# Kernel optimization log

Measured on AMD Instinct MI355X. Metric: run time of the kernel, lower is better.

Reference implementation:

```python
import jax, jax.numpy as jnp
import numpy as np

B, S, D, H, DK, DV = 4, 1024, 1024, 16, 64, 64
NEG = -1e9  # matches torch masked_fill(-1000000000.0)


def setup_inputs() -> dict:
    key = jax.random.key(0)
    ks = jax.random.split(key, 12)
    scale = 1.0 / np.sqrt(D)
    return {
        "querys": jax.random.normal(ks[0], (B, S, D), jnp.float32),
        "keys": jax.random.normal(ks[1], (B, S, D), jnp.float32),
        "values": jax.random.normal(ks[2], (B, S, D), jnp.float32),
        "mask": jax.random.randint(ks[3], (S, S), 0, 2, jnp.int32),
        # stacked per-head projection params (nn.Linear style: y = x @ W^T + b -> here W stored as [D, dk])
        "Wq": jax.random.normal(ks[4], (H, D, DK), jnp.float32) * scale,
        "bq": jax.random.normal(ks[5], (H, DK), jnp.float32) * 0.01,
        "Wk": jax.random.normal(ks[6], (H, D, DK), jnp.float32) * scale,
        "bk": jax.random.normal(ks[7], (H, DK), jnp.float32) * 0.01,
        "Wv": jax.random.normal(ks[8], (H, D, DV), jnp.float32) * scale,
        "bv": jax.random.normal(ks[9], (H, DV), jnp.float32) * 0.01,
        "Wp": jax.random.normal(ks[10], (H * DV, D), jnp.float32) * (1.0 / np.sqrt(H * DV)),
        "bp": jax.random.normal(ks[11], (D,), jnp.float32) * 0.01,
    }


def reference(querys, keys, values, mask, Wq, bq, Wk, bk, Wv, bv, Wp, bp):
    # per-head projections, all heads batched: [B, H, S, dk/dv]
    q = jnp.einsum('bsd,hdk->bhsk', querys, Wq) + bq[None, :, None, :]
    k = jnp.einsum('bsd,hdk->bhsk', keys, Wk) + bk[None, :, None, :]
    v = jnp.einsum('bsd,hdv->bhsv', values, Wv) + bv[None, :, None, :]
    # scores: NO 1/sqrt(dk) scaling, faithful to original broadcast multiply+sum
    scores = jnp.einsum('bhqd,bhkd->bhqk', q, k)  # [B, H, S, S]
    scores = jnp.where(mask[None, None, :, :] == 0, NEG, scores)
    w = jax.nn.softmax(scores, axis=-1)
    o = jnp.einsum('bhqk,bhkv->bhqv', w, v)        # [B, H, S, dv]
    # concat heads along feature dim (head order = H axis), then project
    o = o.transpose(0, 2, 1, 3).reshape(B, S, H * DV)
    return o @ Wp + bp
```

## Files before the change

### kernel.cpp

```cpp
#include <hip/hip_runtime.h>
#include <hip/hip_bf16.h>

typedef unsigned short u16;
typedef unsigned long long u64;
typedef __attribute__((ext_vector_type(4))) float f32x4;
typedef __attribute__((ext_vector_type(8))) __bf16 bf16x8;
typedef __attribute__((ext_vector_type(8))) u16 u16x8;
typedef __attribute__((ext_vector_type(4))) u16 u16x4;

#define DEV __device__ __forceinline__
#define MFMA(a, b, c) __builtin_amdgcn_mfma_f32_16x16x32_bf16(a, b, c, 0, 0, 0)


DEV u16 f2bf(float x) {
  unsigned u = __builtin_bit_cast(unsigned, x);
  u += 0x7fffu + ((u >> 16) & 1u);
  return (u16)(u >> 16);
}
DEV float bf2f(u16 h) {
  unsigned u = ((unsigned)h) << 16;
  return __builtin_bit_cast(float, u);
}
DEV bf16x8 frag8(const u16* p) {
  return __builtin_bit_cast(bf16x8, *(const u16x8*)p);
}

__global__ __launch_bounds__(256) void prep_weights(
    const float* __restrict__ Wq, const float* __restrict__ Wk,
    const float* __restrict__ Wv, const float* __restrict__ Wp,
    u16* __restrict__ wqh, u16* __restrict__ wql,
    u16* __restrict__ wkh, u16* __restrict__ wkl,
    u16* __restrict__ wvh, u16* __restrict__ wph) {
  __shared__ float tile[64][65];
  const int k0 = blockIdx.x * 64;
  const int h = blockIdx.y;
  const int z = blockIdx.z;
  const float* src;
  u16* dhi;
  u16* dlo = nullptr;
  int hs, rs;
  if (z == 0)      { src = Wq; dhi = wqh; dlo = wql; hs = 65536; rs = 64; }
  else if (z == 1) { src = Wk; dhi = wkh; dlo = wkl; hs = 65536; rs = 64; }
  else if (z == 2) { src = Wv; dhi = wvh;            hs = 65536; rs = 64; }
  else             { src = Wp; dhi = wph;            hs = 64;    rs = 1024; }
  const int t = threadIdx.x;
#pragma unroll
  for (int i = 0; i < 16; ++i) {
    int kk = i * 4 + (t >> 6), nn = t & 63;
    tile[kk][nn] = src[h * hs + (k0 + kk) * rs + nn];
  }
  __syncthreads();
#pragma unroll
  for (int i = 0; i < 16; ++i) {
    int nn = i * 4 + (t >> 6), kk = t & 63;
    float x = tile[kk][nn];
    u16 hi = f2bf(x);
    int idx = (h * 64 + nn) * 1024 + k0 + kk;
    dhi[idx] = hi;
    if (dlo) dlo[idx] = f2bf(x - bf2f(hi));
  }
}

__global__ __launch_bounds__(256) void pack_mask(const int* __restrict__ mask,
                                                 u64* __restrict__ mp) {
  int g = blockIdx.x * 4 + (threadIdx.x >> 6);
  int lane = threadIdx.x & 63;
  int v = mask[(g >> 4) * 1024 + (g & 15) * 64 + lane];
  u64 bits = __ballot(v != 0);
  if (lane == 0) mp[g] = bits;
}

template <int MODE>
__global__ __launch_bounds__(256) void proj_kernel(
    const float* __restrict__ X, const u16* __restrict__ Bth,
    const u16* __restrict__ Btl, const float* __restrict__ bias,
    u16* __restrict__ Oh, u16* __restrict__ Ol) {
  __shared__ alignas(16) u16 Ah[128 * 48];
  __shared__ alignas(16) u16 Al[128 * 48];
  __shared__ alignas(16) u16 Bh[128 * 48];
  __shared__ alignas(16) u16 Bl[128 * 48];
  const int m0 = blockIdx.x * 128, n0 = blockIdx.y * 128;
  const int t = threadIdx.x, w = t >> 6, l = t & 63;
  const int wr = w >> 1, wc = w & 1, lr = l & 15, lq = l >> 4;
  f32x4 acc[4][4];
#pragma unroll
  for (int i = 0; i < 4; ++i)
#pragma unroll
    for (int j = 0; j < 4; ++j) acc[i][j] = (f32x4){0.f, 0.f, 0.f, 0.f};

  for (int ks = 0; ks < 32; ++ks) {
    const int k0 = ks * 32;
#pragma unroll
    for (int i = 0; i < 4; ++i) {
      int r = (t >> 3) + i * 32, c = (t & 7) * 4;
      f32x4 v = *(const f32x4*)&X[(m0 + r) * 1024 + k0 + c];
      u16x4 hi, lo;
#pragma unroll
      for (int e = 0; e < 4; ++e) {
        u16 hh = f2bf(v[e]);
        hi[e] = hh;
        lo[e] = f2bf(v[e] - bf2f(hh));
      }
      *(u16x4*)&Ah[r * 48 + c] = hi;
      if constexpr (MODE == 0) *(u16x4*)&Al[r * 48 + c] = lo;
    }
#pragma unroll
    for (int i = 0; i < 2; ++i) {
      int r = (t >> 2) + i * 64, c = (t & 3) * 8;
      *(u16x8*)&Bh[r * 48 + c] = *(const u16x8*)&Bth[(n0 + r) * 1024 + k0 + c];
      if constexpr (MODE == 0)
        *(u16x8*)&Bl[r * 48 + c] = *(const u16x8*)&Btl[(n0 + r) * 1024 + k0 + c];
    }
    __syncthreads();
    bf16x8 ah[4], al[4];
#pragma unroll
    for (int mi = 0; mi < 4; ++mi) {
      int row = wr * 64 + mi * 16 + lr;
      ah[mi] = frag8(&Ah[row * 48 + lq * 8]);
      if constexpr (MODE == 0) al[mi] = frag8(&Al[row * 48 + lq * 8]);
    }
#pragma unroll
    for (int nj = 0; nj < 4; ++nj) {
      int col = wc * 64 + nj * 16 + lr;
      bf16x8 bh = frag8(&Bh[col * 48 + lq * 8]);
      if constexpr (MODE == 0) {
        bf16x8 bl = frag8(&Bl[col * 48 + lq * 8]);
#pragma unroll
        for (int mi = 0; mi < 4; ++mi) {
          acc[mi][nj] = MFMA(ah[mi], bh, acc[mi][nj]);
          acc[mi][nj] = MFMA(ah[mi], bl, acc[mi][nj]);
          acc[mi][nj] = MFMA(al[mi], bh, acc[mi][nj]);
        }
      } else {
#pragma unroll
        for (int mi = 0; mi < 4; ++mi) acc[mi][nj] = MFMA(ah[mi], bh, acc[mi][nj]);
      }
    }
    __syncthreads();
  }
#pragma unroll
  for (int nj = 0; nj < 4; ++nj) {
    int n = n0 + wc * 64 + nj * 16 + lr;
    float bb = bias[n];
    int h = n >> 6, dk = n & 63;
#pragma unroll
    for (int mi = 0; mi < 4; ++mi) {
#pragma unroll
      for (int j = 0; j < 4; ++j) {
        int m = m0 + wr * 64 + mi * 16 + lq * 4 + j;
        int b = m >> 10, s = m & 1023;
        float x = acc[mi][nj][j] + bb;
        if constexpr (MODE == 0) {
          int idx = ((b * 16 + h) * 1024 + s) * 64 + dk;
          u16 hh = f2bf(x);
          Oh[idx] = hh;
          Ol[idx] = f2bf(x - bf2f(hh));
        } else {
          int idx = ((b * 16 + h) * 64 + dk) * 1024 + s;
          Oh[idx] = f2bf(x);
        }
      }
    }
  }
}

__global__ __launch_bounds__(256) void attn_kernel(
    const u16* __restrict__ Qh, const u16* __restrict__ Ql,
    const u16* __restrict__ Kh, const u16* __restrict__ Kl,
    const u16* __restrict__ Vt, const u64* __restrict__ mp,
    u16* __restrict__ Oc) {
  __shared__ alignas(16) u16 Ks_h[64 * 72];
  __shared__ alignas(16) u16 Ks_l[64 * 72];
  __shared__ alignas(16) u16 Vs[64 * 72];
  __shared__ alignas(16) u16 Ps[4][16 * 72];
  __shared__ u64 mw[64];
  const int bid = blockIdx.x;
  const int bh = bid >> 4, qt = bid & 15, q0 = qt * 64;
  const int t = threadIdx.x, w = t >> 6, l = t & 63;
  const int lr = l & 15, lq = l >> 4;
  const int qrow = q0 + w * 16 + lr;

  bf16x8 qh[2], qlo[2];
#pragma unroll
  for (int d = 0; d < 2; ++d) {
    int off = (bh * 1024 + qrow) * 64 + d * 32 + lq * 8;
    qh[d] = frag8(&Qh[off]);
    qlo[d] = frag8(&Ql[off]);
  }
  f32x4 o[4];
#pragma unroll
  for (int dv = 0; dv < 4; ++dv) o[dv] = (f32x4){0.f, 0.f, 0.f, 0.f};
  float mr[4] = {-1e30f, -1e30f, -1e30f, -1e30f};
  float lsum[4] = {0.f, 0.f, 0.f, 0.f};

  for (int kt = 0; kt < 16; ++kt) {
    const int k0 = kt * 64;
    {
      int rr = t >> 2, c0 = (t & 3) * 8;
#pragma unroll
      for (int half = 0; half < 2; ++half) {
        int c = c0 + half * 32;
        *(u16x8*)&Ks_h[rr * 72 + c] = *(const u16x8*)&Kh[(bh * 1024 + k0 + rr) * 64 + c];
        *(u16x8*)&Ks_l[rr * 72 + c] = *(const u16x8*)&Kl[(bh * 1024 + k0 + rr) * 64 + c];
        *(u16x8*)&Vs[rr * 72 + c] = *(const u16x8*)&Vt[(bh * 64 + rr) * 1024 + k0 + c];
      }
      if (t < 64) mw[t] = mp[(q0 + t) * 16 + kt];
    }
    __syncthreads();
    f32x4 s[4];
#pragma unroll
    for (int kb = 0; kb < 4; ++kb) {
      f32x4 a = (f32x4){0.f, 0.f, 0.f, 0.f};
#pragma unroll
      for (int d = 0; d < 2; ++d) {
        bf16x8 kfh = frag8(&Ks_h[(kb * 16 + lr) * 72 + d * 32 + lq * 8]);
        bf16x8 kfl = frag8(&Ks_l[(kb * 16 + lr) * 72 + d * 32 + lq * 8]);
        a = MFMA(qh[d], kfh, a);
        a = MFMA(qh[d], kfl, a);
        a = MFMA(qlo[d], kfh, a);
      }
      s[kb] = a;
    }
#pragma unroll
    for (int j = 0; j < 4; ++j) {
      u64 word = mw[w * 16 + lq * 4 + j];
      float mx = -3e38f;
#pragma unroll
      for (int kb = 0; kb < 4; ++kb) {
        float v = s[kb][j];
        if (!((word >> (kb * 16 + lr)) & 1ull)) v = -1e9f;
        s[kb][j] = v;
        mx = fmaxf(mx, v);
      }
#pragma unroll
      for (int mk = 1; mk < 16; mk <<= 1) mx = fmaxf(mx, __shfl_xor(mx, mk));
      float mn = fmaxf(mr[j], mx);
      float scale = __expf(mr[j] - mn);
      mr[j] = mn;
      float ps = 0.f;
#pragma unroll
      for (int kb = 0; kb < 4; ++kb) {
        float p = __expf(s[kb][j] - mn);
        s[kb][j] = p;
        ps += p;
      }
#pragma unroll
      for (int mk = 1; mk < 16; mk <<= 1) ps += __shfl_xor(ps, mk);
      lsum[j] = lsum[j] * scale + ps;
#pragma unroll
      for (int dv = 0; dv < 4; ++dv) o[dv][j] *= scale;
    }
    u16* pw = &Ps[w][0];
#pragma unroll
    for (int j = 0; j < 4; ++j)
#pragma unroll
      for (int kb = 0; kb < 4; ++kb)
        pw[(lq * 4 + j) * 72 + kb * 16 + lr] = f2bf(s[kb][j]);
#pragma unroll
    for (int kk = 0; kk < 2; ++kk) {
      bf16x8 pa = frag8(&pw[lr * 72 + kk * 32 + lq * 8]);
#pragma unroll
      for (int dv = 0; dv < 4; ++dv) {
        bf16x8 vf = frag8(&Vs[(dv * 16 + lr) * 72 + kk * 32 + lq * 8]);
        o[dv] = MFMA(pa, vf, o[dv]);
      }
    }
    __syncthreads();
  }
  const int b = bh >> 4, h = bh & 15;
#pragma unroll
  for (int j = 0; j < 4; ++j) {
    float inv = 1.f / lsum[j];
    int srow = q0 + w * 16 + lq * 4 + j;
    int base = (b * 1024 + srow) * 1024 + h * 64;
#pragma unroll
    for (int dv = 0; dv < 4; ++dv) Oc[base + dv * 16 + lr] = f2bf(o[dv][j] * inv);
  }
}

__global__ __launch_bounds__(256) void final_kernel(
    const u16* __restrict__ A, const u16* __restrict__ Bt,
    const float* __restrict__ bias, float* __restrict__ out) {
  __shared__ alignas(16) u16 As[128 * 48];
  __shared__ alignas(16) u16 Bs[128 * 48];
  const int m0 = blockIdx.x * 128, n0 = blockIdx.y * 128;
  const int t = threadIdx.x, w = t >> 6, l = t & 63;
  const int wr = w >> 1, wc = w & 1, lr = l & 15, lq = l >> 4;
  f32x4 acc[4][4];
#pragma unroll
  for (int i = 0; i < 4; ++i)
#pragma unroll
    for (int j = 0; j < 4; ++j) acc[i][j] = (f32x4){0.f, 0.f, 0.f, 0.f};

  for (int ks = 0; ks < 32; ++ks) {
    int k0 = ks * 32;
#pragma unroll
    for (int i = 0; i < 2; ++i) {
      int g = t + i * 256;
      int r = g >> 2, c = (g & 3) * 8;
      *(u16x8*)&As[r * 48 + c] = *(const u16x8*)&A[(m0 + r) * 1024 + k0 + c];
      *(u16x8*)&Bs[r * 48 + c] = *(const u16x8*)&Bt[(n0 + r) * 1024 + k0 + c];
    }
    __syncthreads();
    bf16x8 a[4];
#pragma unroll
    for (int mi = 0; mi < 4; ++mi)
      a[mi] = frag8(&As[(wr * 64 + mi * 16 + lr) * 48 + lq * 8]);
#pragma unroll
    for (int nj = 0; nj < 4; ++nj) {
      bf16x8 bfr = frag8(&Bs[(wc * 64 + nj * 16 + lr) * 48 + lq * 8]);
#pragma unroll
      for (int mi = 0; mi < 4; ++mi) acc[mi][nj] = MFMA(a[mi], bfr, acc[mi][nj]);
    }
    __syncthreads();
  }
#pragma unroll
  for (int nj = 0; nj < 4; ++nj) {
    int n = n0 + wc * 64 + nj * 16 + lr;
    float bb = bias[n];
#pragma unroll
    for (int mi = 0; mi < 4; ++mi)
#pragma unroll
      for (int j = 0; j < 4; ++j) {
        int m = m0 + wr * 64 + mi * 16 + lq * 4 + j;
        out[m * 1024 + n] = acc[mi][nj][j] + bb;
      }
  }
}

extern "C" void kernel_launch(void* const* d_in, const int* in_sizes, int n_in,
                              void* d_out, int out_size, void* d_ws, size_t ws_size,
                              hipStream_t stream) {
  (void)in_sizes; (void)n_in; (void)out_size; (void)ws_size;
  const float* querys = (const float*)d_in[0];
  const float* keys = (const float*)d_in[1];
  const float* values = (const float*)d_in[2];
  const int* mask = (const int*)d_in[3];
  const float* Wq = (const float*)d_in[4];
  const float* bq = (const float*)d_in[5];
  const float* Wk = (const float*)d_in[6];
  const float* bk = (const float*)d_in[7];
  const float* Wv = (const float*)d_in[8];
  const float* bv = (const float*)d_in[9];
  const float* Wp = (const float*)d_in[10];
  const float* bp = (const float*)d_in[11];
  float* out = (float*)d_out;

  char* ws = (char*)d_ws;
  const size_t MB = 1024ull * 1024ull;
  u16* Qh = (u16*)(ws + 0 * MB);
  u16* Ql = (u16*)(ws + 8 * MB);
  u16* Kh = (u16*)(ws + 16 * MB);
  u16* Kl = (u16*)(ws + 24 * MB);
  u16* Vt = (u16*)(ws + 32 * MB);
  u16* Oc = (u16*)(ws + 40 * MB);
  u16* wqh = (u16*)(ws + 48 * MB);
  u16* wql = (u16*)(ws + 50 * MB);
  u16* wkh = (u16*)(ws + 52 * MB);
  u16* wkl = (u16*)(ws + 54 * MB);
  u16* wvh = (u16*)(ws + 56 * MB);
  u16* wph = (u16*)(ws + 58 * MB);
  u64* mp = (u64*)(ws + 60 * MB);

  prep_weights<<<dim3(16, 16, 4), 256, 0, stream>>>(Wq, Wk, Wv, Wp, wqh, wql, wkh,
                                                    wkl, wvh, wph);
  pack_mask<<<dim3(4096), 256, 0, stream>>>(mask, mp);
  proj_kernel<0><<<dim3(32, 8), 256, 0, stream>>>(querys, wqh, wql, bq, Qh, Ql);
  proj_kernel<0><<<dim3(32, 8), 256, 0, stream>>>(keys, wkh, wkl, bk, Kh, Kl);
  proj_kernel<1><<<dim3(32, 8), 256, 0, stream>>>(values, wvh, nullptr, bv, Vt, nullptr);
  attn_kernel<<<dim3(1024), 256, 0, stream>>>(Qh, Ql, Kh, Kl, Vt, mp, Oc);
  final_kernel<<<dim3(32, 8), 256, 0, stream>>>(Oc, wph, bp, out);
}
```

Before: 374.1 us.

## Fuse QKV projections, prefetch attention tiles, shrink final GEMM tile

Result: no change. 370.2 us (-1.0%).

```diff
diff --git a/kernel.cpp b/kernel.cpp
--- a/kernel.cpp
+++ b/kernel.cpp
@@ -70,15 +70,27 @@
   if (lane == 0) mp[g] = bits;
 }
 
-template <int MODE>
-__global__ __launch_bounds__(256) void proj_kernel(
-    const float* __restrict__ X, const u16* __restrict__ Bth,
-    const u16* __restrict__ Btl, const float* __restrict__ bias,
-    u16* __restrict__ Oh, u16* __restrict__ Ol) {
+__global__ __launch_bounds__(256, 3) void proj_fused(
+    const float* __restrict__ Xq, const float* __restrict__ Xk,
+    const float* __restrict__ Xv, const u16* __restrict__ wqh,
+    const u16* __restrict__ wql, const u16* __restrict__ wkh,
+    const u16* __restrict__ wkl, const u16* __restrict__ wvh,
+    const float* __restrict__ bq, const float* __restrict__ bk,
+    const float* __restrict__ bv, u16* __restrict__ Qh, u16* __restrict__ Ql,
+    u16* __restrict__ Kh, u16* __restrict__ Kl, u16* __restrict__ Vt) {
   __shared__ alignas(16) u16 Ah[128 * 48];
   __shared__ alignas(16) u16 Al[128 * 48];
   __shared__ alignas(16) u16 Bh[128 * 48];
   __shared__ alignas(16) u16 Bl[128 * 48];
+  const int z = blockIdx.z;
+  const bool split = (z < 2);
+  const float* X = (z == 0) ? Xq : (z == 1) ? Xk : Xv;
+  const u16* Bth = (z == 0) ? wqh : (z == 1) ? wkh : wvh;
+  const u16* Btl = (z == 0) ? wql : wkl;
+  const float* bias = (z == 0) ? bq : (z == 1) ? bk : bv;
+  u16* Oh = (z == 0) ? Qh : (z == 1) ? Kh : Vt;
+  u16* Ol = (z == 0) ? Ql : Kl;
+
   const int m0 = blockIdx.x * 128, n0 = blockIdx.y * 128;
   const int t = threadIdx.x, w = t >> 6, l = t & 63;
   const int wr = w >> 1, wc = w & 1, lr = l & 15, lq = l >> 4;
@@ -102,13 +114,13 @@
         lo[e] = f2bf(v[e] - bf2f(hh));
       }
       *(u16x4*)&Ah[r * 48 + c] = hi;
-      if constexpr (MODE == 0) *(u16x4*)&Al[r * 48 + c] = lo;
+      if (split) *(u16x4*)&Al[r * 48 + c] = lo;
     }
 #pragma unroll
     for (int i = 0; i < 2; ++i) {
       int r = (t >> 2) + i * 64, c = (t & 3) * 8;
       *(u16x8*)&Bh[r * 48 + c] = *(const u16x8*)&Bth[(n0 + r) * 1024 + k0 + c];
-      if constexpr (MODE == 0)
+      if (split)
         *(u16x8*)&Bl[r * 48 + c] = *(const u16x8*)&Btl[(n0 + r) * 1024 + k0 + c];
     }
     __syncthreads();
@@ -117,13 +129,13 @@
     for (int mi = 0; mi < 4; ++mi) {
       int row = wr * 64 + mi * 16 + lr;
       ah[mi] = frag8(&Ah[row * 48 + lq * 8]);
-      if constexpr (MODE == 0) al[mi] = frag8(&Al[row * 48 + lq * 8]);
-    }
-#pragma unroll
-    for (int nj = 0; nj < 4; ++nj) {
-      int col = wc * 64 + nj * 16 + lr;
-      bf16x8 bh = frag8(&Bh[col * 48 + lq * 8]);
-      if constexpr (MODE == 0) {
+      if (split) al[mi] = frag8(&Al[row * 48 + lq * 8]);
+    }
+    if (split) {
+#pragma unroll
+      for (int nj = 0; nj < 4; ++nj) {
+        int col = wc * 64 + nj * 16 + lr;
+        bf16x8 bh = frag8(&Bh[col * 48 + lq * 8]);
         bf16x8 bl = frag8(&Bl[col * 48 + lq * 8]);
 #pragma unroll
         for (int mi = 0; mi < 4; ++mi) {
@@ -131,7 +143,12 @@
           acc[mi][nj] = MFMA(ah[mi], bl, acc[mi][nj]);
           acc[mi][nj] = MFMA(al[mi], bh, acc[mi][nj]);
         }
-      } else {
+      }
+    } else {
+#pragma unroll
+      for (int nj = 0; nj < 4; ++nj) {
+        int col = wc * 64 + nj * 16 + lr;
+        bf16x8 bh = frag8(&Bh[col * 48 + lq * 8]);
 #pragma unroll
         for (int mi = 0; mi < 4; ++mi) acc[mi][nj] = MFMA(ah[mi], bh, acc[mi][nj]);
       }
@@ -150,7 +167,7 @@
         int m = m0 + wr * 64 + mi * 16 + lq * 4 + j;
         int b = m >> 10, s = m & 1023;
         float x = acc[mi][nj][j] + bb;
-        if constexpr (MODE == 0) {
+        if (split) {
           int idx = ((b * 16 + h) * 1024 + s) * 64 + dk;
           u16 hh = f2bf(x);
           Oh[idx] = hh;
@@ -164,7 +181,7 @@
   }
 }
 
-__global__ __launch_bounds__(256) void attn_kernel(
+__global__ __launch_bounds__(256, 4) void attn_kernel(
     const u16* __restrict__ Qh, const u16* __restrict__ Ql,
     const u16* __restrict__ Kh, const u16* __restrict__ Kl,
     const u16* __restrict__ Vt, const u64* __restrict__ mp,
@@ -179,6 +196,7 @@
   const int t = threadIdx.x, w = t >> 6, l = t & 63;
   const int lr = l & 15, lq = l >> 4;
   const int qrow = q0 + w * 16 + lr;
+  const int rr = t >> 2, c0 = (t & 3) * 8;
 
   bf16x8 qh[2], qlo[2];
 #pragma unroll
@@ -193,20 +211,32 @@
   float mr[4] = {-1e30f, -1e30f, -1e30f, -1e30f};
   float lsum[4] = {0.f, 0.f, 0.f, 0.f};
 
+  u16x8 rKh[2], rKl[2], rVs[2];
+  u64 rMw = 0;
+  auto issue = [&](int kt) {
+    const int k0 = kt * 64;
+#pragma unroll
+    for (int half = 0; half < 2; ++half) {
+      int c = c0 + half * 32;
+      rKh[half] = *(const u16x8*)&Kh[(bh * 1024 + k0 + rr) * 64 + c];
+      rKl[half] = *(const u16x8*)&Kl[(bh * 1024 + k0 + rr) * 64 + c];
+      rVs[half] = *(const u16x8*)&Vt[(bh * 64 + rr) * 1024 + k0 + c];
+    }
+    if (t < 64) rMw = mp[(q0 + t) * 16 + kt];
+  };
+
+  issue(0);
   for (int kt = 0; kt < 16; ++kt) {
-    const int k0 = kt * 64;
-    {
-      int rr = t >> 2, c0 = (t & 3) * 8;
-#pragma unroll
-      for (int half = 0; half < 2; ++half) {
-        int c = c0 + half * 32;
-        *(u16x8*)&Ks_h[rr * 72 + c] = *(const u16x8*)&Kh[(bh * 1024 + k0 + rr) * 64 + c];
-        *(u16x8*)&Ks_l[rr * 72 + c] = *(const u16x8*)&Kl[(bh * 1024 + k0 + rr) * 64 + c];
-        *(u16x8*)&Vs[rr * 72 + c] = *(const u16x8*)&Vt[(bh * 64 + rr) * 1024 + k0 + c];
-      }
-      if (t < 64) mw[t] = mp[(q0 + t) * 16 + kt];
-    }
-    __syncthreads();
+#pragma unroll
+    for (int half = 0; half < 2; ++half) {
+      int c = c0 + half * 32;
+      *(u16x8*)&Ks_h[rr * 72 + c] = rKh[half];
+      *(u16x8*)&Ks_l[rr * 72 + c] = rKl[half];
+      *(u16x8*)&Vs[rr * 72 + c] = rVs[half];
+    }
+    if (t < 64) mw[t] = rMw;
+    __syncthreads();
+    if (kt < 15) issue(kt + 1);
     f32x4 s[4];
 #pragma unroll
     for (int kb = 0; kb < 4; ++kb) {
@@ -281,36 +311,38 @@
 __global__ __launch_bounds__(256) void final_kernel(
     const u16* __restrict__ A, const u16* __restrict__ Bt,
     const float* __restrict__ bias, float* __restrict__ out) {
-  __shared__ alignas(16) u16 As[128 * 48];
+  __shared__ alignas(16) u16 As[64 * 48];
   __shared__ alignas(16) u16 Bs[128 * 48];
-  const int m0 = blockIdx.x * 128, n0 = blockIdx.y * 128;
+  const int m0 = blockIdx.x * 64, n0 = blockIdx.y * 128;
   const int t = threadIdx.x, w = t >> 6, l = t & 63;
   const int wr = w >> 1, wc = w & 1, lr = l & 15, lq = l >> 4;
-  f32x4 acc[4][4];
-#pragma unroll
-  for (int i = 0; i < 4; ++i)
+  f32x4 acc[2][4];
+#pragma unroll
+  for (int i = 0; i < 2; ++i)
 #pragma unroll
     for (int j = 0; j < 4; ++j) acc[i][j] = (f32x4){0.f, 0.f, 0.f, 0.f};
 
   for (int ks = 0; ks < 32; ++ks) {
     int k0 = ks * 32;
-#pragma unroll
-    for (int i = 0; i < 2; ++i) {
-      int g = t + i * 256;
-      int r = g >> 2, c = (g & 3) * 8;
+    {
+      int r = t >> 2, c = (t & 3) * 8;
       *(u16x8*)&As[r * 48 + c] = *(const u16x8*)&A[(m0 + r) * 1024 + k0 + c];
-      *(u16x8*)&Bs[r * 48 + c] = *(const u16x8*)&Bt[(n0 + r) * 1024 + k0 + c];
-    }
-    __syncthreads();
-    bf16x8 a[4];
-#pragma unroll
-    for (int mi = 0; mi < 4; ++mi)
-      a[mi] = frag8(&As[(wr * 64 + mi * 16 + lr) * 48 + lq * 8]);
+#pragma unroll
+      for (int i = 0; i < 2; ++i) {
+        int rb = r + i * 64;
+        *(u16x8*)&Bs[rb * 48 + c] = *(const u16x8*)&Bt[(n0 + rb) * 1024 + k0 + c];
+      }
+    }
+    __syncthreads();
+    bf16x8 a[2];
+#pragma unroll
+    for (int mi = 0; mi < 2; ++mi)
+      a[mi] = frag8(&As[(wr * 32 + mi * 16 + lr) * 48 + lq * 8]);
 #pragma unroll
     for (int nj = 0; nj < 4; ++nj) {
       bf16x8 bfr = frag8(&Bs[(wc * 64 + nj * 16 + lr) * 48 + lq * 8]);
 #pragma unroll
-      for (int mi = 0; mi < 4; ++mi) acc[mi][nj] = MFMA(a[mi], bfr, acc[mi][nj]);
+      for (int mi = 0; mi < 2; ++mi) acc[mi][nj] = MFMA(a[mi], bfr, acc[mi][nj]);
     }
     __syncthreads();
   }
@@ -319,10 +351,10 @@
     int n = n0 + wc * 64 + nj * 16 + lr;
     float bb = bias[n];
 #pragma unroll
-    for (int mi = 0; mi < 4; ++mi)
+    for (int mi = 0; mi < 2; ++mi)
 #pragma unroll
       for (int j = 0; j < 4; ++j) {
-        int m = m0 + wr * 64 + mi * 16 + lq * 4 + j;
+        int m = m0 + wr * 32 + mi * 16 + lq * 4 + j;
         out[m * 1024 + n] = acc[mi][nj][j] + bb;
       }
   }
@@ -365,9 +397,9 @@
   prep_weights<<<dim3(16, 16, 4), 256, 0, stream>>>(Wq, Wk, Wv, Wp, wqh, wql, wkh,
                                                     wkl, wvh, wph);
   pack_mask<<<dim3(4096), 256, 0, stream>>>(mask, mp);
-  proj_kernel<0><<<dim3(32, 8), 256, 0, stream>>>(querys, wqh, wql, bq, Qh, Ql);
-  proj_kernel<0><<<dim3(32, 8), 256, 0, stream>>>(keys, wkh, wkl, bk, Kh, Kl);
-  proj_kernel<1><<<dim3(32, 8), 256, 0, stream>>>(values, wvh, nullptr, bv, Vt, nullptr);
+  proj_fused<<<dim3(32, 8, 3), 256, 0, stream>>>(querys, keys, values, wqh, wql,
+                                                 wkh, wkl, wvh, bq, bk, bv, Qh, Ql,
+                                                 Kh, Kl, Vt);
   attn_kernel<<<dim3(1024), 256, 0, stream>>>(Qh, Ql, Kh, Kl, Vt, mp, Oc);
-  final_kernel<<<dim3(32, 8), 256, 0, stream>>>(Oc, wph, bp, out);
-}
+  final_kernel<<<dim3(64, 8), 256, 0, stream>>>(Oc, wph, bp, out);
+}
```
